# Optimization experiments

Measured on AMD Instinct MI355X. Metric: run time of the kernel, lower is better.

## Reference

```python
import jax, jax.numpy as jnp
import numpy as np

B, N, D, L, V, E = 16, 512, 512, 4, 128, 131072
PAD = 127

def setup_inputs() -> dict:
    key = jax.random.key(0)
    ks = jax.random.split(key, 16)
    src_tokens = jax.random.randint(ks[0], (B, N), 0, PAD)  # 0..126, never PAD
    padded_coordinates = jax.random.normal(ks[1], (B, N, 3), dtype=jnp.float32)
    src_distance = jax.random.uniform(ks[2], (B, N, N), dtype=jnp.float32)
    src_edge_type = jax.random.randint(ks[3], (B, N, N), 0, 16)
    edge_index = jax.random.randint(ks[4], (2, E), 0, B * N)
    s = 0.02
    embed_tokens = jax.random.normal(ks[5], (V, D), dtype=jnp.float32) * s
    embed_tokens = embed_tokens.at[PAD].set(0.0)  # nn.Embedding padding_idx row is zero
    vec_proj_w = jax.random.normal(ks[6], (3, D), dtype=jnp.float32) * s
    vec_proj_b = jnp.zeros((D,), dtype=jnp.float32)
    Wq = jax.random.normal(ks[7], (L, D, D), dtype=jnp.float32) * s
    bq = jnp.zeros((L, D), dtype=jnp.float32)
    Wkv = jax.random.normal(ks[8], (L, D, 3 * D), dtype=jnp.float32) * s
    bkv = jnp.zeros((L, 3 * D), dtype=jnp.float32)
    Wvm = jax.random.normal(ks[9], (L, D, D), dtype=jnp.float32) * s
    bvm = jnp.zeros((L, D), dtype=jnp.float32)
    return dict(src_tokens=src_tokens, padded_coordinates=padded_coordinates,
                src_distance=src_distance, src_edge_type=src_edge_type,
                edge_index=edge_index, embed_tokens=embed_tokens,
                vec_proj_w=vec_proj_w, vec_proj_b=vec_proj_b,
                Wq=Wq, bq=bq, Wkv=Wkv, bkv=bkv, Wvm=Wvm, bvm=bvm)

def reference(src_tokens, padded_coordinates, src_distance, src_edge_type,
              edge_index, embed_tokens, vec_proj_w, vec_proj_b,
              Wq, bq, Wkv, bkv, Wvm, bvm):
    padding_mask = src_tokens == PAD                      # [B,N] (all False here)
    x = embed_tokens[src_tokens].reshape(B * N, D)        # [BN,D]
    coord = padded_coordinates.reshape(B * N, 3)          # [BN,3]
    v = coord @ vec_proj_w + vec_proj_b                   # [BN,D]
    row, col = edge_index[0], edge_index[1]               # [E]
    for l in range(L):
        q = x @ Wq[l] + bq[l]                             # [BN,D]
        kv = x @ Wkv[l] + bkv[l]                          # [BN,3D]
        k, v_s, v_v = jnp.split(kv, 3, axis=-1)
        ew = jnp.sum(q[row] * k[col], axis=-1, keepdims=True)   # [E,1] edge score
        msg_s = ew * v_s[col]                             # [E,D]
        msg_v = ew * v_v[col] * v[col]                    # [E,D] gated vector message
        agg_s = jnp.zeros_like(x).at[row].add(msg_s)      # scatter-add to dest nodes
        agg_v = jnp.zeros_like(v).at[row].add(msg_v)
        x = x + agg_s
        v = v + (agg_v @ Wvm[l] + bvm[l])
    out = jnp.where(padding_mask.reshape(-1, 1), 0.0, x).reshape(B, N, D)
    return out, padding_mask
```

## Files before the change

### kernel.cpp

```cpp
#include <hip/hip_runtime.h>
#include <hip/hip_bf16.h>

#define NNODE 8192
#define DIM 512
#define NEDGE 131072
#define NLAYER 4
#define PADIDX 127

typedef float4 f4;
typedef __attribute__((ext_vector_type(8))) short s16x8;
typedef __attribute__((ext_vector_type(4))) float f32x4;

static __device__ __forceinline__ float bf2f(unsigned short h){
  return __uint_as_float(((unsigned int)h) << 16);
}
static __device__ __forceinline__ unsigned short f2bf(float f){
  unsigned int u = __float_as_uint(f);
  u += 0x7FFFu + ((u >> 16) & 1u);
  return (unsigned short)(u >> 16);
}
static __device__ __forceinline__ float blo(unsigned int u){ return __uint_as_float(u << 16); }
static __device__ __forceinline__ float bhi(unsigned int u){ return __uint_as_float(u & 0xFFFF0000u); }
static __device__ __forceinline__ unsigned int pack2(float a, float b){
  return (unsigned int)f2bf(a) | ((unsigned int)f2bf(b) << 16);
}

__global__ void k_detect(const unsigned short* __restrict__ src, int* __restrict__ flag){
  int lane = threadIdx.x;
  float v = bf2f(src[2*lane]);
  float a = fabsf(v);
  bool good = (a > 1e-6f) && (a < 0.5f);
  unsigned long long m = __ballot(good);
  if (lane == 0) *flag = (__popcll(m) >= 32) ? 1 : 0;
}

__global__ void k_convert(const void* __restrict__ src, float* __restrict__ dst, int n,
                          const int* __restrict__ flag){
  int f = *flag;
  int i = blockIdx.x*blockDim.x + threadIdx.x;
  int stride = gridDim.x*blockDim.x;
  if (f){
    const unsigned short* s = (const unsigned short*)src;
    for (; i<n; i+=stride) dst[i] = bf2f(s[i]);
  } else {
    const float* s = (const float*)src;
    for (; i<n; i+=stride) dst[i] = s[i];
  }
}

__global__ void k_convT(const void* __restrict__ src, unsigned short* __restrict__ dst,
                        int C, int dstOff, int dstStride, const int* __restrict__ flag){
  int f = *flag;
  int i = blockIdx.x*blockDim.x + threadIdx.x;
  if (i >= 512*C) return;
  int r = i & 511;
  int c = i >> 9;
  size_t si = (size_t)blockIdx.z*512*C + (size_t)r*C + c;
  unsigned short o;
  if (f) o = ((const unsigned short*)src)[si];
  else   o = f2bf(((const float*)src)[si]);
  dst[(size_t)blockIdx.z*dstStride + (size_t)(dstOff + c)*512 + r] = o;
}

__global__ void k_bias(const void* __restrict__ bq, const void* __restrict__ bkv,
                       float* __restrict__ dst, const int* __restrict__ flag){
  int f = *flag;
  int gid = blockIdx.x*blockDim.x + threadIdx.x;
  if (gid >= NLAYER*2048) return;
  int l = gid >> 11, j = gid & 2047;
  float val;
  if (j < 512)
    val = f ? bf2f(((const unsigned short*)bq)[l*512+j]) : ((const float*)bq)[l*512+j];
  else
    val = f ? bf2f(((const unsigned short*)bkv)[l*1536 + j-512]) : ((const float*)bkv)[l*1536 + j-512];
  dst[gid] = val;
}

__global__ void k_zero_i(int* __restrict__ p, int n){
  int i = blockIdx.x*blockDim.x + threadIdx.x;
  if (i<n) p[i]=0;
}

__global__ void k_count(const int* __restrict__ row, int* __restrict__ counts){
  int e = blockIdx.x*blockDim.x + threadIdx.x;
  if (e<NEDGE) atomicAdd(&counts[row[e]], 1);
}

__global__ __launch_bounds__(1024) void k_scan(const int* __restrict__ counts,
                                               int* __restrict__ offs, int* __restrict__ cursor){
  __shared__ int part[1024];
  int tid = threadIdx.x;
  int local[8]; int s = 0;
  #pragma unroll
  for (int j=0;j<8;j++){ local[j]=s; s += counts[tid*8+j]; }
  part[tid]=s;
  __syncthreads();
  for (int off=1; off<1024; off<<=1){
    int t = (tid>=off) ? part[tid-off] : 0;
    __syncthreads();
    part[tid] += t;
    __syncthreads();
  }
  int base = (tid>0) ? part[tid-1] : 0;
  #pragma unroll
  for (int j=0;j<8;j++){ int o = base + local[j]; offs[tid*8+j]=o; cursor[tid*8+j]=o; }
  if (tid==1023) offs[8192] = part[1023];
}

__global__ void k_fill(const int* __restrict__ ei, int* __restrict__ cursor, int* __restrict__ ecol){
  int e = blockIdx.x*blockDim.x + threadIdx.x;
  if (e<NEDGE){ int p = atomicAdd(&cursor[ei[e]], 1); ecol[p] = ei[NEDGE+e]; }
}

__global__ void k_init(const int* __restrict__ tok, const void* __restrict__ emb,
                       const void* __restrict__ coord, const void* __restrict__ vw,
                       const void* __restrict__ vb, const int* __restrict__ flag,
                       float* __restrict__ x, float* __restrict__ v,
                       unsigned short* __restrict__ xbf){
  int f = *flag;
  int i = blockIdx.x*blockDim.x + threadIdx.x;
  if (i >= NNODE*DIM) return;
  int n = i >> 9, d = i & 511;
  int t = tok[n];
  float xv, c0, c1, c2, w0, w1, w2, bb;
  if (f){
    const unsigned short* e = (const unsigned short*)emb;
    const unsigned short* c = (const unsigned short*)coord;
    const unsigned short* wv = (const unsigned short*)vw;
    const unsigned short* bv = (const unsigned short*)vb;
    xv = bf2f(e[(t<<9)|d]);
    c0 = bf2f(c[n*3+0]); c1 = bf2f(c[n*3+1]); c2 = bf2f(c[n*3+2]);
    w0 = bf2f(wv[d]); w1 = bf2f(wv[512+d]); w2 = bf2f(wv[1024+d]);
    bb = bf2f(bv[d]);
  } else {
    const float* e = (const float*)emb;
    const float* c = (const float*)coord;
    const float* wv = (const float*)vw;
    const float* bv = (const float*)vb;
    xv = e[(t<<9)|d];
    c0 = c[n*3+0]; c1 = c[n*3+1]; c2 = c[n*3+2];
    w0 = wv[d]; w1 = wv[512+d]; w2 = wv[1024+d];
    bb = bv[d];
  }
  x[i] = xv;
  xbf[i] = f2bf(xv);
  v[i] = c0*w0 + c1*w1 + c2*w2 + bb;
}

#define BM 128
#define BN 128
#define BK 64

static __device__ __forceinline__ void gload16(const void* g, void* l){
  __builtin_amdgcn_global_load_lds(
      (const __attribute__((address_space(1))) void*)g,
      (__attribute__((address_space(3))) void*)l, 16, 0, 0);
}

__global__ __launch_bounds__(256) void k_mgemm(const unsigned short* __restrict__ A,
                                               const unsigned short* __restrict__ Bt,
                                               const float* __restrict__ bias,
                                               void* __restrict__ C,
                                               int ldc, int mode){
  __shared__ alignas(16) unsigned short As[2][BM*BK];
  __shared__ alignas(16) unsigned short Bs[2][BN*BK];
  int tid  = threadIdx.x;
  int lane = tid & 63;
  int w    = tid >> 6;
  int wr   = (w >> 1) * 64;
  int wc   = (w & 1) * 64;
  int bm   = blockIdx.y * BM;
  int bn   = blockIdx.x * BN;

  f32x4 acc[4][4];
  #pragma unroll
  for (int m=0;m<4;m++)
    #pragma unroll
    for (int n=0;n<4;n++) acc[m][n] = (f32x4){0.f,0.f,0.f,0.f};

  int srow = tid >> 3;
  int sp   = tid & 7;

  auto STAGE = [&](int b, int kt){
    char* AsB = (char*)As[b];
    char* BsB = (char*)Bs[b];
    #pragma unroll
    for (int i=0;i<4;i++){
      int row  = i*32 + srow;
      int slot = sp ^ (row & 7);
      gload16((const char*)A + (((size_t)(bm + row)) << 10) + (size_t)((kt + slot*8) << 1),
              AsB + i*4096 + w*1024);
    }
    #pragma unroll
    for (int i=0;i<4;i++){
      int row  = i*32 + srow;
      int slot = sp ^ (row & 7);
      gload16((const char*)Bt + (((size_t)(bn + row)) << 10) + (size_t)((kt + slot*8) << 1),
              BsB + i*4096 + w*1024);
    }
  };

  STAGE(0, 0);
  __syncthreads();

  for (int it = 0; it < 8; ++it){
    if (it < 7) STAGE((it+1)&1, (it+1)*BK);
    const char* AsB = (const char*)As[it&1];
    const char* BsB = (const char*)Bs[it&1];

    s16x8 af[4][2], bfr[4][2];
    #pragma unroll
    for (int m=0;m<4;m++){
      int row = wr + m*16 + (lane & 15);
      #pragma unroll
      for (int kk=0;kk<2;kk++){
        int slot = kk*4 + (lane >> 4);
        af[m][kk] = *(const s16x8*)(AsB + row*128 + ((slot ^ (row & 7)) << 4));
      }
    }
    #pragma unroll
    for (int n=0;n<4;n++){
      int row = wc + n*16 + (lane & 15);
      #pragma unroll
      for (int kk=0;kk<2;kk++){
        int slot = kk*4 + (lane >> 4);
        bfr[n][kk] = *(const s16x8*)(BsB + row*128 + ((slot ^ (row & 7)) << 4));
      }
    }
    #pragma unroll
    for (int kk=0;kk<2;kk++)
      #pragma unroll
      for (int m=0;m<4;m++)
        #pragma unroll
        for (int n=0;n<4;n++)
          acc[m][n] = __builtin_amdgcn_mfma_f32_16x16x32_bf16(af[m][kk], bfr[n][kk], acc[m][n], 0, 0, 0);

    if (it < 7) __syncthreads();
  }

  int colb = bn + wc + (lane & 15);
  int rowb = bm + wr + ((lane >> 4) << 2);
  float bb[4];
  #pragma unroll
  for (int n=0;n<4;n++) bb[n] = bias[colb + n*16];
  #pragma unroll
  for (int m=0;m<4;m++){
    #pragma unroll
    for (int n=0;n<4;n++){
      #pragma unroll
      for (int j=0;j<4;j++){
        size_t o = (size_t)(rowb + m*16 + j)*ldc + (colb + n*16);
        float val = acc[m][n][j] + bb[n];
        if (mode == 2)      ((unsigned short*)C)[o] = f2bf(val);
        else if (mode == 1) ((float*)C)[o] += val;
        else                ((float*)C)[o] = val;
      }
    }
  }
}

__global__ void k_vvip(unsigned short* __restrict__ qkv, const float* __restrict__ v){
  int gid = blockIdx.x*blockDim.x + threadIdx.x;
  int n = gid >> 6, d8 = (gid & 63) * 8;
  unsigned short* p = qkv + (size_t)n*2048 + 1536 + d8;
  uint4 u = *(uint4*)p;
  f4 v0 = *(const f4*)(v + (size_t)n*512 + d8);
  f4 v1 = *(const f4*)(v + (size_t)n*512 + d8 + 4);
  uint4 o;
  o.x = pack2(blo(u.x)*v0.x, bhi(u.x)*v0.y);
  o.y = pack2(blo(u.y)*v0.z, bhi(u.y)*v0.w);
  o.z = pack2(blo(u.z)*v1.x, bhi(u.z)*v1.y);
  o.w = pack2(blo(u.w)*v1.z, bhi(u.w)*v1.w);
  *(uint4*)p = o;
}

__global__ __launch_bounds__(256) void k_fused(const int* __restrict__ offs,
                                               const int* __restrict__ ecol,
                                               const unsigned short* __restrict__ qkv,
                                               float* __restrict__ x,
                                               unsigned short* __restrict__ xbf,
                                               unsigned short* __restrict__ aggvbf){
  __shared__ unsigned short qs[512];
  __shared__ float ews[64];
  __shared__ int cols[64];
  int n = blockIdx.x, tid = threadIdx.x;
  int beg = offs[n], end = offs[n+1];
  if (tid < 64)
    *(uint4*)&qs[tid*8] = *(const uint4*)(qkv + (size_t)n*2048 + tid*8);
  float a0=0.f, a1=0.f, a2=0.f, a3=0.f;
  int half = tid >> 7;
  int d4 = (tid & 127) * 4;
  size_t srcoff = half ? 1536 : 1024;
  int lane = tid & 63, w = tid >> 6;

  for (int cb = beg; cb < end; cb += 64){
    int cnt = min(64, end - cb);
    __syncthreads();
    for (int j = w; j < cnt; j += 4){
      int c = ecol[cb + j];
      uint4 ku = *(const uint4*)(qkv + (size_t)c*2048 + 512 + lane*8);
      uint4 qu = *(const uint4*)(qs + lane*8);
      float s = blo(qu.x)*blo(ku.x) + bhi(qu.x)*bhi(ku.x)
              + blo(qu.y)*blo(ku.y) + bhi(qu.y)*bhi(ku.y)
              + blo(qu.z)*blo(ku.z) + bhi(qu.z)*bhi(ku.z)
              + blo(qu.w)*blo(ku.w) + bhi(qu.w)*bhi(ku.w);
      #pragma unroll
      for (int o=32;o;o>>=1) s += __shfl_xor(s, o, 64);
      if (lane == 0){ ews[j] = s; cols[j] = c; }
    }
    __syncthreads();
    #pragma unroll 2
    for (int j = 0; j < cnt; j++){
      float wgt = ews[j];
      int c = cols[j];
      uint2 u = *(const uint2*)(qkv + (size_t)c*2048 + srcoff + d4);
      a0 += wgt*blo(u.x); a1 += wgt*bhi(u.x);
      a2 += wgt*blo(u.y); a3 += wgt*bhi(u.y);
    }
  }

  size_t base = (size_t)n*512 + d4;
  if (half == 0){
    f4 xv = *(const f4*)(x + base);
    xv.x += a0; xv.y += a1; xv.z += a2; xv.w += a3;
    *(f4*)(x + base) = xv;
    uint2 o; o.x = pack2(xv.x, xv.y); o.y = pack2(xv.z, xv.w);
    *(uint2*)(xbf + base) = o;
  } else {
    uint2 o; o.x = pack2(a0, a1); o.y = pack2(a2, a3);
    *(uint2*)(aggvbf + base) = o;
  }
}

__global__ void k_out(const int* __restrict__ tok, const float* __restrict__ x,
                      float* __restrict__ out, int out_size){
  int i = blockIdx.x*blockDim.x + threadIdx.x;
  if (i>=out_size) return;
  if (i < NNODE*DIM){
    int n = i>>9;
    out[i] = (tok[n]==PADIDX) ? 0.f : x[i];
  } else {
    int m = i - NNODE*DIM;
    out[i] = (m < NNODE && tok[m]==PADIDX) ? 1.f : 0.f;
  }
}

extern "C" void kernel_launch(void* const* d_in, const int* in_sizes, int n_in,
                              void* d_out, int out_size, void* d_ws, size_t ws_size,
                              hipStream_t stream){
  (void)in_sizes; (void)n_in; (void)ws_size;
  const int*  tok   = (const int*)d_in[0];
  const void* coord = d_in[1];
  const int*  ei    = (const int*)d_in[4];
  const void* emb   = d_in[5];
  const void* vpw   = d_in[6];
  const void* vpb   = d_in[7];
  const void* Wq    = d_in[8];
  const void* bq    = d_in[9];
  const void* Wkv   = d_in[10];
  const void* bkv   = d_in[11];
  const void* Wvm   = d_in[12];
  const void* bvm   = d_in[13];

  char* p = (char*)d_ws;
  auto alloc = [&](size_t nbytes)->char*{ char* r = p; p += (nbytes + 255) & ~(size_t)255; return r; };
  float* x      = (float*)alloc((size_t)NNODE*DIM*4);
  float* v      = (float*)alloc((size_t)NNODE*DIM*4);
  unsigned short* qkv    = (unsigned short*)alloc((size_t)NNODE*2048*2);
  unsigned short* xbf    = (unsigned short*)alloc((size_t)NNODE*DIM*2);
  unsigned short* aggvbf = (unsigned short*)alloc((size_t)NNODE*DIM*2);
  unsigned short* WqkvT  = (unsigned short*)alloc((size_t)NLAYER*2048*DIM*2);
  unsigned short* WvmT   = (unsigned short*)alloc((size_t)NLAYER*DIM*DIM*2);
  float* cbqkv  = (float*)alloc((size_t)NLAYER*2048*4);
  float* cbvm   = (float*)alloc((size_t)NLAYER*DIM*4);
  int* counts   = (int*)alloc(8192*4);
  int* offs     = (int*)alloc(8193*4);
  int* cursor   = (int*)alloc(8192*4);
  int* ecol     = (int*)alloc((size_t)NEDGE*4);
  int* flag     = (int*)alloc(4);

  k_detect<<<1,64,0,stream>>>((const unsigned short*)Wq, flag);
  k_convert<<<8,256,0,stream>>>(bvm, cbvm, NLAYER*DIM, flag);
  k_bias<<<(NLAYER*2048+255)/256,256,0,stream>>>(bq, bkv, cbqkv, flag);
  k_convT<<<dim3((512*512+255)/256,1,NLAYER),256,0,stream>>>(Wq,  WqkvT, 512,  0,   2048*512, flag);
  k_convT<<<dim3((512*1536+255)/256,1,NLAYER),256,0,stream>>>(Wkv, WqkvT, 1536, 512, 2048*512, flag);
  k_convT<<<dim3((512*512+255)/256,1,NLAYER),256,0,stream>>>(Wvm, WvmT,  512,  0,   512*512,  flag);

  k_zero_i<<<32,256,0,stream>>>(counts, 8192);
  k_count<<<NEDGE/256,256,0,stream>>>(ei, counts);
  k_scan<<<1,1024,0,stream>>>(counts, offs, cursor);
  k_fill<<<NEDGE/256,256,0,stream>>>(ei, cursor, ecol);

  k_init<<<(NNODE*DIM)/256,256,0,stream>>>(tok, emb, coord, vpw, vpb, flag, x, v, xbf);

  for (int l=0;l<NLAYER;l++){
    const unsigned short* WqkvT_l = WqkvT + (size_t)l*2048*DIM;
    const unsigned short* WvmT_l  = WvmT  + (size_t)l*DIM*DIM;
    const float* bqkv_l = cbqkv + (size_t)l*2048;
    const float* bvm_l  = cbvm  + (size_t)l*DIM;
    k_mgemm<<<dim3(2048/BN, NNODE/BM),256,0,stream>>>(xbf, WqkvT_l, bqkv_l, qkv, 2048, 2);
    k_vvip<<<NNODE*64/256,256,0,stream>>>(qkv, v);
    k_fused<<<NNODE,256,0,stream>>>(offs, ecol, qkv, x, xbf, aggvbf);
    k_mgemm<<<dim3(DIM/BN, NNODE/BM),256,0,stream>>>(aggvbf, WvmT_l, bvm_l, v, 512, 1);
  }

  int ob = (out_size+255)/256;
  k_out<<<ob,256,0,stream>>>(tok, x, (float*)d_out, out_size);
}
```

Measured before the change: 697.5 us.

## Tile weight transpose via LDS, drop LDS staging in GEMM, batch gather loads

```diff
diff --git a/kernel.cpp b/kernel.cpp
--- a/kernel.cpp
+++ b/kernel.cpp
@@ -50,16 +50,25 @@
 
 __global__ void k_convT(const void* __restrict__ src, unsigned short* __restrict__ dst,
                         int C, int dstOff, int dstStride, const int* __restrict__ flag){
+  __shared__ unsigned short t[64][65];
   int f = *flag;
-  int i = blockIdx.x*blockDim.x + threadIdx.x;
-  if (i >= 512*C) return;
-  int r = i & 511;
-  int c = i >> 9;
-  size_t si = (size_t)blockIdx.z*512*C + (size_t)r*C + c;
-  unsigned short o;
-  if (f) o = ((const unsigned short*)src)[si];
-  else   o = f2bf(((const float*)src)[si]);
-  dst[(size_t)blockIdx.z*dstStride + (size_t)(dstOff + c)*512 + r] = o;
+  int c0 = blockIdx.x*64, r0 = blockIdx.y*64;
+  size_t mat = (size_t)blockIdx.z*512*C;
+  int tx = threadIdx.x & 63, ty = threadIdx.x >> 6;
+  #pragma unroll
+  for (int i=0;i<16;i++){
+    int r = ty + i*4;
+    size_t si = mat + (size_t)(r0+r)*C + c0 + tx;
+    unsigned short o = f ? ((const unsigned short*)src)[si] : f2bf(((const float*)src)[si]);
+    t[tx][r] = o;
+  }
+  __syncthreads();
+  size_t dbase = (size_t)blockIdx.z*dstStride;
+  #pragma unroll
+  for (int i=0;i<16;i++){
+    int c = ty + i*4;
+    dst[dbase + (size_t)(dstOff + c0 + c)*512 + r0 + tx] = t[c][tx];
+  }
 }
 
 __global__ void k_bias(const void* __restrict__ bq, const void* __restrict__ bkv,
@@ -149,21 +158,12 @@
 
 #define BM 128
 #define BN 128
-#define BK 64
-
-static __device__ __forceinline__ void gload16(const void* g, void* l){
-  __builtin_amdgcn_global_load_lds(
-      (const __attribute__((address_space(1))) void*)g,
-      (__attribute__((address_space(3))) void*)l, 16, 0, 0);
-}
 
 __global__ __launch_bounds__(256) void k_mgemm(const unsigned short* __restrict__ A,
                                                const unsigned short* __restrict__ Bt,
                                                const float* __restrict__ bias,
                                                void* __restrict__ C,
                                                int ldc, int mode){
-  __shared__ alignas(16) unsigned short As[2][BM*BK];
-  __shared__ alignas(16) unsigned short Bs[2][BN*BK];
   int tid  = threadIdx.x;
   int lane = tid & 63;
   int w    = tid >> 6;
@@ -172,61 +172,29 @@
   int bm   = blockIdx.y * BM;
   int bn   = blockIdx.x * BN;
 
+  int arow = bm + wr + (lane & 15);
+  int brow = bn + wc + (lane & 15);
+  int ksl  = lane >> 4;
+
   f32x4 acc[4][4];
   #pragma unroll
   for (int m=0;m<4;m++)
     #pragma unroll
     for (int n=0;n<4;n++) acc[m][n] = (f32x4){0.f,0.f,0.f,0.f};
 
-  int srow = tid >> 3;
-  int sp   = tid & 7;
-
-  auto STAGE = [&](int b, int kt){
-    char* AsB = (char*)As[b];
-    char* BsB = (char*)Bs[b];
-    #pragma unroll
-    for (int i=0;i<4;i++){
-      int row  = i*32 + srow;
-      int slot = sp ^ (row & 7);
-      gload16((const char*)A + (((size_t)(bm + row)) << 10) + (size_t)((kt + slot*8) << 1),
-              AsB + i*4096 + w*1024);
-    }
-    #pragma unroll
-    for (int i=0;i<4;i++){
-      int row  = i*32 + srow;
-      int slot = sp ^ (row & 7);
-      gload16((const char*)Bt + (((size_t)(bn + row)) << 10) + (size_t)((kt + slot*8) << 1),
-              BsB + i*4096 + w*1024);
-    }
-  };
-
-  STAGE(0, 0);
-  __syncthreads();
-
-  for (int it = 0; it < 8; ++it){
-    if (it < 7) STAGE((it+1)&1, (it+1)*BK);
-    const char* AsB = (const char*)As[it&1];
-    const char* BsB = (const char*)Bs[it&1];
-
+  #pragma unroll 2
+  for (int kt = 0; kt < 512; kt += 64){
     s16x8 af[4][2], bfr[4][2];
     #pragma unroll
-    for (int m=0;m<4;m++){
-      int row = wr + m*16 + (lane & 15);
-      #pragma unroll
-      for (int kk=0;kk<2;kk++){
-        int slot = kk*4 + (lane >> 4);
-        af[m][kk] = *(const s16x8*)(AsB + row*128 + ((slot ^ (row & 7)) << 4));
-      }
-    }
-    #pragma unroll
-    for (int n=0;n<4;n++){
-      int row = wc + n*16 + (lane & 15);
-      #pragma unroll
-      for (int kk=0;kk<2;kk++){
-        int slot = kk*4 + (lane >> 4);
-        bfr[n][kk] = *(const s16x8*)(BsB + row*128 + ((slot ^ (row & 7)) << 4));
-      }
-    }
+    for (int m=0;m<4;m++)
+      #pragma unroll
+      for (int kk=0;kk<2;kk++)
+        af[m][kk] = *(const s16x8*)(A + (size_t)(arow + m*16)*512 + kt + (kk*4 + ksl)*8);
+    #pragma unroll
+    for (int n=0;n<4;n++)
+      #pragma unroll
+      for (int kk=0;kk<2;kk++)
+        bfr[n][kk] = *(const s16x8*)(Bt + (size_t)(brow + n*16)*512 + kt + (kk*4 + ksl)*8);
     #pragma unroll
     for (int kk=0;kk<2;kk++)
       #pragma unroll
@@ -234,8 +202,6 @@
         #pragma unroll
         for (int n=0;n<4;n++)
           acc[m][n] = __builtin_amdgcn_mfma_f32_16x16x32_bf16(af[m][kk], bfr[n][kk], acc[m][n], 0, 0, 0);
-
-    if (it < 7) __syncthreads();
   }
 
   int colb = bn + wc + (lane & 15);
@@ -296,24 +262,44 @@
   for (int cb = beg; cb < end; cb += 64){
     int cnt = min(64, end - cb);
     __syncthreads();
-    for (int j = w; j < cnt; j += 4){
-      int c = ecol[cb + j];
-      uint4 ku = *(const uint4*)(qkv + (size_t)c*2048 + 512 + lane*8);
-      uint4 qu = *(const uint4*)(qs + lane*8);
-      float s = blo(qu.x)*blo(ku.x) + bhi(qu.x)*bhi(ku.x)
-              + blo(qu.y)*blo(ku.y) + bhi(qu.y)*bhi(ku.y)
-              + blo(qu.z)*blo(ku.z) + bhi(qu.z)*bhi(ku.z)
-              + blo(qu.w)*blo(ku.w) + bhi(qu.w)*bhi(ku.w);
-      #pragma unroll
-      for (int o=32;o;o>>=1) s += __shfl_xor(s, o, 64);
-      if (lane == 0){ ews[j] = s; cols[j] = c; }
+    uint4 qu = *(const uint4*)(qs + lane*8);
+    for (int t0 = 0; t0 < 16 && w + 4*t0 < cnt; t0 += 4){
+      int cc[4]; uint4 ku[4];
+      #pragma unroll
+      for (int s=0;s<4;s++){ int j = w + 4*(t0+s); cc[s] = (j < cnt) ? ecol[cb+j] : 0; }
+      #pragma unroll
+      for (int s=0;s<4;s++){ int j = w + 4*(t0+s);
+        if (j < cnt) ku[s] = *(const uint4*)(qkv + (size_t)cc[s]*2048 + 512 + lane*8); }
+      #pragma unroll
+      for (int s=0;s<4;s++){
+        int j = w + 4*(t0+s);
+        if (j < cnt){
+          float sd = blo(qu.x)*blo(ku[s].x) + bhi(qu.x)*bhi(ku[s].x)
+                   + blo(qu.y)*blo(ku[s].y) + bhi(qu.y)*bhi(ku[s].y)
+                   + blo(qu.z)*blo(ku[s].z) + bhi(qu.z)*bhi(ku[s].z)
+                   + blo(qu.w)*blo(ku[s].w) + bhi(qu.w)*bhi(ku[s].w);
+          #pragma unroll
+          for (int o=32;o;o>>=1) sd += __shfl_xor(sd, o, 64);
+          if (lane == 0){ ews[j] = sd; cols[j] = cc[s]; }
+        }
+      }
     }
     __syncthreads();
-    #pragma unroll 2
-    for (int j = 0; j < cnt; j++){
+    int j = 0;
+    for (; j + 8 <= cnt; j += 8){
+      float wg[8]; uint2 u[8];
+      #pragma unroll
+      for (int t=0;t<8;t++){ wg[t] = ews[j+t];
+        u[t] = *(const uint2*)(qkv + (size_t)cols[j+t]*2048 + srcoff + d4); }
+      #pragma unroll
+      for (int t=0;t<8;t++){
+        a0 += wg[t]*blo(u[t].x); a1 += wg[t]*bhi(u[t].x);
+        a2 += wg[t]*blo(u[t].y); a3 += wg[t]*bhi(u[t].y);
+      }
+    }
+    for (; j < cnt; j++){
       float wgt = ews[j];
-      int c = cols[j];
-      uint2 u = *(const uint2*)(qkv + (size_t)c*2048 + srcoff + d4);
+      uint2 u = *(const uint2*)(qkv + (size_t)cols[j]*2048 + srcoff + d4);
       a0 += wgt*blo(u.x); a1 += wgt*bhi(u.x);
       a2 += wgt*blo(u.y); a3 += wgt*bhi(u.y);
     }
@@ -382,9 +368,9 @@
   k_detect<<<1,64,0,stream>>>((const unsigned short*)Wq, flag);
   k_convert<<<8,256,0,stream>>>(bvm, cbvm, NLAYER*DIM, flag);
   k_bias<<<(NLAYER*2048+255)/256,256,0,stream>>>(bq, bkv, cbqkv, flag);
-  k_convT<<<dim3((512*512+255)/256,1,NLAYER),256,0,stream>>>(Wq,  WqkvT, 512,  0,   2048*512, flag);
-  k_convT<<<dim3((512*1536+255)/256,1,NLAYER),256,0,stream>>>(Wkv, WqkvT, 1536, 512, 2048*512, flag);
-  k_convT<<<dim3((512*512+255)/256,1,NLAYER),256,0,stream>>>(Wvm, WvmT,  512,  0,   512*512,  flag);
+  k_convT<<<dim3(8, 8, NLAYER),256,0,stream>>>(Wq,  WqkvT, 512,  0,   2048*512, flag);
+  k_convT<<<dim3(24,8, NLAYER),256,0,stream>>>(Wkv, WqkvT, 1536, 512, 2048*512, flag);
+  k_convT<<<dim3(8, 8, NLAYER),256,0,stream>>>(Wvm, WvmT,  512,  0,   512*512,  flag);
 
   k_zero_i<<<32,256,0,stream>>>(counts, 8192);
   k_count<<<NEDGE/256,256,0,stream>>>(ei, counts);
```

Result: slower. 863.5 us (+23.8%).

## Tile weight transpose, single-buffer GEMM, and restructure edge aggregation per warp

Applied to the files above, without the earlier changes.

```diff
diff --git a/kernel.cpp b/kernel.cpp
--- a/kernel.cpp
+++ b/kernel.cpp
@@ -50,16 +50,25 @@
 
 __global__ void k_convT(const void* __restrict__ src, unsigned short* __restrict__ dst,
                         int C, int dstOff, int dstStride, const int* __restrict__ flag){
+  __shared__ unsigned short t[64][65];
   int f = *flag;
-  int i = blockIdx.x*blockDim.x + threadIdx.x;
-  if (i >= 512*C) return;
-  int r = i & 511;
-  int c = i >> 9;
-  size_t si = (size_t)blockIdx.z*512*C + (size_t)r*C + c;
-  unsigned short o;
-  if (f) o = ((const unsigned short*)src)[si];
-  else   o = f2bf(((const float*)src)[si]);
-  dst[(size_t)blockIdx.z*dstStride + (size_t)(dstOff + c)*512 + r] = o;
+  int c0 = blockIdx.x*64, r0 = blockIdx.y*64;
+  size_t mat = (size_t)blockIdx.z*512*C;
+  int tx = threadIdx.x & 63, ty = threadIdx.x >> 6;
+  #pragma unroll
+  for (int i=0;i<16;i++){
+    int r = ty + i*4;
+    size_t si = mat + (size_t)(r0+r)*C + c0 + tx;
+    unsigned short o = f ? ((const unsigned short*)src)[si] : f2bf(((const float*)src)[si]);
+    t[tx][r] = o;
+  }
+  __syncthreads();
+  size_t dbase = (size_t)blockIdx.z*dstStride;
+  #pragma unroll
+  for (int i=0;i<16;i++){
+    int c = ty + i*4;
+    dst[dbase + (size_t)(dstOff + c0 + c)*512 + r0 + tx] = t[c][tx];
+  }
 }
 
 __global__ void k_bias(const void* __restrict__ bq, const void* __restrict__ bkv,
@@ -162,8 +171,8 @@
                                                const float* __restrict__ bias,
                                                void* __restrict__ C,
                                                int ldc, int mode){
-  __shared__ alignas(16) unsigned short As[2][BM*BK];
-  __shared__ alignas(16) unsigned short Bs[2][BN*BK];
+  __shared__ alignas(16) unsigned short As[BM*BK];
+  __shared__ alignas(16) unsigned short Bs[BN*BK];
   int tid  = threadIdx.x;
   int lane = tid & 63;
   int w    = tid >> 6;
@@ -180,10 +189,11 @@
 
   int srow = tid >> 3;
   int sp   = tid & 7;
-
-  auto STAGE = [&](int b, int kt){
-    char* AsB = (char*)As[b];
-    char* BsB = (char*)Bs[b];
+  char* AsB = (char*)As;
+  char* BsB = (char*)Bs;
+
+  for (int kt = 0; kt < 512; kt += BK){
+    if (kt) __syncthreads();
     #pragma unroll
     for (int i=0;i<4;i++){
       int row  = i*32 + srow;
@@ -198,15 +208,7 @@
       gload16((const char*)Bt + (((size_t)(bn + row)) << 10) + (size_t)((kt + slot*8) << 1),
               BsB + i*4096 + w*1024);
     }
-  };
-
-  STAGE(0, 0);
-  __syncthreads();
-
-  for (int it = 0; it < 8; ++it){
-    if (it < 7) STAGE((it+1)&1, (it+1)*BK);
-    const char* AsB = (const char*)As[it&1];
-    const char* BsB = (const char*)Bs[it&1];
+    __syncthreads();
 
     s16x8 af[4][2], bfr[4][2];
     #pragma unroll
@@ -234,8 +236,6 @@
         #pragma unroll
         for (int n=0;n<4;n++)
           acc[m][n] = __builtin_amdgcn_mfma_f32_16x16x32_bf16(af[m][kk], bfr[n][kk], acc[m][n], 0, 0, 0);
-
-    if (it < 7) __syncthreads();
   }
 
   int colb = bn + wc + (lane & 15);
@@ -280,56 +280,74 @@
                                                float* __restrict__ x,
                                                unsigned short* __restrict__ xbf,
                                                unsigned short* __restrict__ aggvbf){
-  __shared__ unsigned short qs[512];
-  __shared__ float ews[64];
-  __shared__ int cols[64];
+  __shared__ float redS[4][512];
+  __shared__ float redV[4][512];
   int n = blockIdx.x, tid = threadIdx.x;
+  int lane = tid & 63, w = tid >> 6;
   int beg = offs[n], end = offs[n+1];
-  if (tid < 64)
-    *(uint4*)&qs[tid*8] = *(const uint4*)(qkv + (size_t)n*2048 + tid*8);
-  float a0=0.f, a1=0.f, a2=0.f, a3=0.f;
-  int half = tid >> 7;
-  int d4 = (tid & 127) * 4;
-  size_t srcoff = half ? 1536 : 1024;
-  int lane = tid & 63, w = tid >> 6;
-
-  for (int cb = beg; cb < end; cb += 64){
-    int cnt = min(64, end - cb);
-    __syncthreads();
-    for (int j = w; j < cnt; j += 4){
-      int c = ecol[cb + j];
-      uint4 ku = *(const uint4*)(qkv + (size_t)c*2048 + 512 + lane*8);
-      uint4 qu = *(const uint4*)(qs + lane*8);
-      float s = blo(qu.x)*blo(ku.x) + bhi(qu.x)*bhi(ku.x)
-              + blo(qu.y)*blo(ku.y) + bhi(qu.y)*bhi(ku.y)
-              + blo(qu.z)*blo(ku.z) + bhi(qu.z)*bhi(ku.z)
-              + blo(qu.w)*blo(ku.w) + bhi(qu.w)*bhi(ku.w);
-      #pragma unroll
-      for (int o=32;o;o>>=1) s += __shfl_xor(s, o, 64);
-      if (lane == 0){ ews[j] = s; cols[j] = c; }
-    }
-    __syncthreads();
-    #pragma unroll 2
-    for (int j = 0; j < cnt; j++){
-      float wgt = ews[j];
-      int c = cols[j];
-      uint2 u = *(const uint2*)(qkv + (size_t)c*2048 + srcoff + d4);
-      a0 += wgt*blo(u.x); a1 += wgt*bhi(u.x);
-      a2 += wgt*blo(u.y); a3 += wgt*bhi(u.y);
-    }
-  }
-
-  size_t base = (size_t)n*512 + d4;
-  if (half == 0){
-    f4 xv = *(const f4*)(x + base);
-    xv.x += a0; xv.y += a1; xv.z += a2; xv.w += a3;
-    *(f4*)(x + base) = xv;
-    uint2 o; o.x = pack2(xv.x, xv.y); o.y = pack2(xv.z, xv.w);
-    *(uint2*)(xbf + base) = o;
-  } else {
-    uint2 o; o.x = pack2(a0, a1); o.y = pack2(a2, a3);
-    *(uint2*)(aggvbf + base) = o;
-  }
+
+  uint4 qu = *(const uint4*)(qkv + (size_t)n*2048 + lane*8);
+  float as[8], av[8];
+  #pragma unroll
+  for (int k=0;k<8;k++){ as[k]=0.f; av[k]=0.f; }
+
+  auto edge = [&](int c, uint4 ku, uint4 vs, uint4 vv){
+    float sd = blo(qu.x)*blo(ku.x) + bhi(qu.x)*bhi(ku.x)
+             + blo(qu.y)*blo(ku.y) + bhi(qu.y)*bhi(ku.y)
+             + blo(qu.z)*blo(ku.z) + bhi(qu.z)*bhi(ku.z)
+             + blo(qu.w)*blo(ku.w) + bhi(qu.w)*bhi(ku.w);
+    #pragma unroll
+    for (int o=32;o;o>>=1) sd += __shfl_xor(sd, o, 64);
+    as[0] += sd*blo(vs.x); as[1] += sd*bhi(vs.x);
+    as[2] += sd*blo(vs.y); as[3] += sd*bhi(vs.y);
+    as[4] += sd*blo(vs.z); as[5] += sd*bhi(vs.z);
+    as[6] += sd*blo(vs.w); as[7] += sd*bhi(vs.w);
+    av[0] += sd*blo(vv.x); av[1] += sd*bhi(vv.x);
+    av[2] += sd*blo(vv.y); av[3] += sd*bhi(vv.y);
+    av[4] += sd*blo(vv.z); av[5] += sd*bhi(vv.z);
+    av[6] += sd*blo(vv.w); av[7] += sd*bhi(vv.w);
+  };
+
+  int j = beg + w;
+  for (; j + 4 < end; j += 8){
+    int c0 = ecol[j], c1 = ecol[j+4];
+    const unsigned short* b0 = qkv + (size_t)c0*2048;
+    const unsigned short* b1 = qkv + (size_t)c1*2048;
+    uint4 ku0 = *(const uint4*)(b0 + 512  + lane*8);
+    uint4 ku1 = *(const uint4*)(b1 + 512  + lane*8);
+    uint4 vs0 = *(const uint4*)(b0 + 1024 + lane*8);
+    uint4 vv0 = *(const uint4*)(b0 + 1536 + lane*8);
+    uint4 vs1 = *(const uint4*)(b1 + 1024 + lane*8);
+    uint4 vv1 = *(const uint4*)(b1 + 1536 + lane*8);
+    edge(c0, ku0, vs0, vv0);
+    edge(c1, ku1, vs1, vv1);
+  }
+  if (j < end){
+    int c0 = ecol[j];
+    const unsigned short* b0 = qkv + (size_t)c0*2048;
+    uint4 ku0 = *(const uint4*)(b0 + 512  + lane*8);
+    uint4 vs0 = *(const uint4*)(b0 + 1024 + lane*8);
+    uint4 vv0 = *(const uint4*)(b0 + 1536 + lane*8);
+    edge(c0, ku0, vs0, vv0);
+  }
+
+  #pragma unroll
+  for (int k=0;k<8;k+=4){
+    *(f4*)&redS[w][lane*8+k] = (f4){as[k],as[k+1],as[k+2],as[k+3]};
+    *(f4*)&redV[w][lane*8+k] = (f4){av[k],av[k+1],av[k+2],av[k+3]};
+  }
+  __syncthreads();
+  int d0 = tid*2;
+  float s0 = redS[0][d0]+redS[1][d0]+redS[2][d0]+redS[3][d0];
+  float s1 = redS[0][d0+1]+redS[1][d0+1]+redS[2][d0+1]+redS[3][d0+1];
+  float v0 = redV[0][d0]+redV[1][d0]+redV[2][d0]+redV[3][d0];
+  float v1 = redV[0][d0+1]+redV[1][d0+1]+redV[2][d0+1]+redV[3][d0+1];
+  size_t base = (size_t)n*512 + d0;
+  float2 xv = *(const float2*)(x + base);
+  xv.x += s0; xv.y += s1;
+  *(float2*)(x + base) = xv;
+  ((unsigned int*)xbf)[base>>1]    = pack2(xv.x, xv.y);
+  ((unsigned int*)aggvbf)[base>>1] = pack2(v0, v1);
 }
 
 __global__ void k_out(const int* __restrict__ tok, const float* __restrict__ x,
@@ -382,9 +400,9 @@
   k_detect<<<1,64,0,stream>>>((const unsigned short*)Wq, flag);
   k_convert<<<8,256,0,stream>>>(bvm, cbvm, NLAYER*DIM, flag);
   k_bias<<<(NLAYER*2048+255)/256,256,0,stream>>>(bq, bkv, cbqkv, flag);
-  k_convT<<<dim3((512*512+255)/256,1,NLAYER),256,0,stream>>>(Wq,  WqkvT, 512,  0,   2048*512, flag);
-  k_convT<<<dim3((512*1536+255)/256,1,NLAYER),256,0,stream>>>(Wkv, WqkvT, 1536, 512, 2048*512, flag);
-  k_convT<<<dim3((512*512+255)/256,1,NLAYER),256,0,stream>>>(Wvm, WvmT,  512,  0,   512*512,  flag);
+  k_convT<<<dim3(8, 8, NLAYER),256,0,stream>>>(Wq,  WqkvT, 512,  0,   2048*512, flag);
+  k_convT<<<dim3(24,8, NLAYER),256,0,stream>>>(Wkv, WqkvT, 1536, 512, 2048*512, flag);
+  k_convT<<<dim3(8, 8, NLAYER),256,0,stream>>>(Wvm, WvmT,  512,  0,   512*512,  flag);
 
   k_zero_i<<<32,256,0,stream>>>(counts, 8192);
   k_count<<<NEDGE/256,256,0,stream>>>(ei, counts);
```

Result: faster. 674.0 us (-3.4%).
